# Optimization experiments

Hardware: AMD Instinct MI355X
Metric: run time of the kernel (lower is better)

The kernel has to match this reference:

```python
import jax, jax.numpy as jnp
import numpy as np


def setup_inputs() -> dict:
    key = jax.random.key(0)
    k1, k2, k3, k4 = jax.random.split(key, 4)
    b, c_in, t, h, w = 8, 64, 16, 64, 64
    c_out, kh, kw = 64, 3, 3
    x = jax.random.normal(k1, (b, c_in, t, h, w), dtype=jnp.float32)
    alpha = jax.random.uniform(k2, (b, c_in, t, 1, 1), dtype=jnp.float32)
    fan_in = c_in * kh * kw
    weight = jax.random.normal(k3, (c_out, c_in, kh, kw), dtype=jnp.float32) / np.sqrt(fan_in)
    bias = jax.random.normal(k4, (c_out,), dtype=jnp.float32) * 0.05
    return {"x": x, "alpha": alpha, "weight": weight, "bias": bias}


def reference(x, alpha, weight, bias):
    # x: (b, c_in, t, h, w); alpha: (b, c_in, t, 1, 1)
    # weight: (c_out, c_in, kh, kw); bias: (c_out,)
    b, c_in, t, h, w = x.shape
    c_out, _, kh, kw = weight.shape
    pad = ((kh // 2, kh // 2), (kw // 2, kw // 2))  # padding=1 for 3x3
    # per-(b,t) calibrated weights: alpha scales the c_in dim (cal_dim='cin')
    a = jnp.transpose(alpha[..., 0, 0], (0, 2, 1))          # (b, t, c_in)
    w_bt = a[:, :, None, :, None, None] * weight[None, None]  # (b, t, c_out, c_in, kh, kw)
    xs = jnp.transpose(x, (0, 2, 1, 3, 4)).reshape(b * t, 1, c_in, h, w)
    ws = w_bt.reshape(b * t, c_out, c_in, kh, kw)

    def conv_one(xi, wi):
        return jax.lax.conv_general_dilated(
            xi, wi, window_strides=(1, 1), padding=pad,
            dimension_numbers=("NCHW", "OIHW", "NCHW"))[0]

    out = jax.vmap(conv_one)(xs, ws)                          # (b*t, c_out, h, w)
    out = out + bias[None, :, None, None]
    out = out.reshape(b, t, c_out, h, w).transpose(0, 2, 1, 3, 4)
    return out  # (b, c_out, t, h, w)
```

## Files before the change

kernel.cpp:

```cpp
#include <hip/hip_runtime.h>


#define CIN  64
#define COUT 64
#define TT   16
#define BB   8
#define HH   64
#define WW   64

typedef __attribute__((ext_vector_type(8))) short bf16x8;
typedef __attribute__((ext_vector_type(4))) float f32x4;

__device__ __forceinline__ unsigned short f2bf(float f) {
    union { float f; unsigned u; } v; v.f = f;
    unsigned r = (v.u + 0x7FFF + ((v.u >> 16) & 1)) >> 16;
    return (unsigned short)r;
}

__global__ __launch_bounds__(256) void prep_w(const float* __restrict__ wgt,
                                              unsigned short* __restrict__ wb) {
    int idx = blockIdx.x * 256 + threadIdx.x;
    if (idx < COUT * CIN * 9) {
        int co  = idx / (CIN * 9);
        int r   = idx - co * (CIN * 9);
        int ci  = r / 9;
        int tap = r - ci * 9;
        int slot = (ci >> 3) ^ (co & 7);
        wb[((tap * COUT + co) * 8 + slot) * 8 + (ci & 7)] = f2bf(wgt[idx]);
    }
}

__global__ __launch_bounds__(512, 4) void conv3(const float* __restrict__ x,
                                                const float* __restrict__ alpha,
                                                const short* __restrict__ wb,
                                                const float* __restrict__ bias,
                                                float* __restrict__ out) {
    __shared__ __align__(16) short xs[6][66 * 64];
    __shared__ __align__(16) short wl[2][64 * 64];

    const int orig  = blockIdx.x;
    const int blk   = (orig & 7) * 256 + (orig >> 3);
    const int ytile = blk & 15;
    const int bt    = blk >> 4;
    const int t     = bt & 15;
    const int b     = bt >> 4;
    const int y0    = ytile * 4;
    const int tid   = threadIdx.x;
    const int wv    = tid >> 6;
    const int lane  = tid & 63;

    {
        const int cib = wv * 8;
        float a0 = alpha[(b * CIN + cib + 0) * TT + t];
        float a1 = alpha[(b * CIN + cib + 1) * TT + t];
        float a2 = alpha[(b * CIN + cib + 2) * TT + t];
        float a3 = alpha[(b * CIN + cib + 3) * TT + t];
        float a4 = alpha[(b * CIN + cib + 4) * TT + t];
        float a5 = alpha[(b * CIN + cib + 5) * TT + t];
        float a6 = alpha[(b * CIN + cib + 6) * TT + t];
        float a7 = alpha[(b * CIN + cib + 7) * TT + t];
        const float* xb = x + (size_t)((b * CIN + cib) * TT + t) * (HH * WW);
        const int slot = wv ^ (lane & 7);
        const int CI_STRIDE = TT * HH * WW;
#pragma unroll
        for (int r = 0; r < 6; ++r) {
            const int gy = y0 - 1 + r;
            int4 o = {0, 0, 0, 0};
            if ((unsigned)gy < HH) {
                const float* p = xb + gy * WW + lane;
                float v0 = p[0 * CI_STRIDE] * a0;
                float v1 = p[1 * CI_STRIDE] * a1;
                float v2 = p[2 * CI_STRIDE] * a2;
                float v3 = p[3 * CI_STRIDE] * a3;
                float v4 = p[4 * CI_STRIDE] * a4;
                float v5 = p[5 * CI_STRIDE] * a5;
                float v6 = p[6 * CI_STRIDE] * a6;
                float v7 = p[7 * CI_STRIDE] * a7;
                o.x = (int)f2bf(v0) | ((int)f2bf(v1) << 16);
                o.y = (int)f2bf(v2) | ((int)f2bf(v3) << 16);
                o.z = (int)f2bf(v4) | ((int)f2bf(v5) << 16);
                o.w = (int)f2bf(v6) | ((int)f2bf(v7) << 16);
            }
            *(int4*)(xs[r] + (lane + 1) * 64 + slot * 8) = o;
            if (lane < 2) {
                int4 z = {0, 0, 0, 0};
                *(int4*)(xs[r] + lane * 65 * 64 + wv * 8) = z;
            }
        }
    }
    ((int4*)wl[0])[tid] = ((const int4*)wb)[tid];
    __syncthreads();

    f32x4 acc[4][2] = {};
    const int ywave = wv >> 1;
    const int wseg  = (wv & 1) * 32;
    const int co_l  = lane & 15;
    const int kg    = lane >> 4;

    for (int tap = 0; tap < 9; ++tap) {
        const int cur = tap & 1;
        int4 wp;
        if (tap < 8)
            wp = ((const int4*)(wb + (tap + 1) * 4096))[tid];
        const int ky = tap / 3;
        const int dx = (tap - 3 * ky) - 1;
        const short* xrow = xs[ywave + ky];
        const short* wcur = wl[cur];

#pragma unroll
        for (int kc = 0; kc < 2; ++kc) {
            const int g = kc * 4 + kg;
            bf16x8 af[4];
#pragma unroll
            for (int m = 0; m < 4; ++m) {
                int co   = m * 16 + co_l;
                int slot = g ^ (co & 7);
                af[m] = *(const bf16x8*)(wcur + co * 64 + slot * 8);
            }
            bf16x8 bfr[2];
#pragma unroll
            for (int nt = 0; nt < 2; ++nt) {
                int w    = wseg + nt * 16 + co_l;
                int wx   = w + dx;
                int slot = g ^ (wx & 7);
                bfr[nt] = *(const bf16x8*)(xrow + (wx + 1) * 64 + slot * 8);
            }
#pragma unroll
            for (int m = 0; m < 4; ++m)
#pragma unroll
                for (int nt = 0; nt < 2; ++nt)
                    acc[m][nt] = __builtin_amdgcn_mfma_f32_16x16x32_bf16(
                        af[m], bfr[nt], acc[m][nt], 0, 0, 0);
        }

        if (tap < 8)
            ((int4*)wl[cur ^ 1])[tid] = wp;
        __syncthreads();
    }

    const int y = y0 + ywave;
#pragma unroll
    for (int m = 0; m < 4; ++m) {
#pragma unroll
        for (int r = 0; r < 4; ++r) {
            int co = m * 16 + kg * 4 + r;
            float bv = bias[co];
            float* op = out + (size_t)(((b * COUT + co) * TT + t) * HH + y) * WW;
#pragma unroll
            for (int nt = 0; nt < 2; ++nt) {
                int w = wseg + nt * 16 + co_l;
                op[w] = acc[m][nt][r] + bv;
            }
        }
    }
}

extern "C" void kernel_launch(void* const* d_in, const int* in_sizes, int n_in,
                              void* d_out, int out_size, void* d_ws, size_t ws_size,
                              hipStream_t stream) {
    const float* x      = (const float*)d_in[0];
    const float* alpha  = (const float*)d_in[1];
    const float* weight = (const float*)d_in[2];
    const float* bias   = (const float*)d_in[3];
    float* out          = (float*)d_out;

    unsigned short* wb = (unsigned short*)d_ws;

    hipLaunchKernelGGL(prep_w, dim3(144), dim3(256), 0, stream, weight, wb);
    hipLaunchKernelGGL(conv3, dim3(BB * TT * (HH / 4)), dim3(512), 0, stream,
                       x, alpha, (const short*)wb, bias, out);
}
```

Baseline: 261.2 us.

## Hold per-wave weight fragments in registers and drop the LDS weight pipeline

Weights are repacked in MFMA fragment order, and each wave now owns one 16-output-channel quarter. It loads all 9 taps of its weight fragments into registers once, so the per-tap LDS weight double buffer and its nine barriers go away. The wave-to-output mapping changes from 4 co-tiles × 2 w-tiles to 1 co-tile × 2 rows × 4 w-tiles, so the main loop only reads activations from LDS. This costs 72 extra VGPRs per thread for the weights, which may strain the 4-blocks-per-CU launch bound or cause spills.

```diff
diff --git a/kernel.cpp b/kernel.cpp
--- a/kernel.cpp
+++ b/kernel.cpp
@@ -25,18 +25,21 @@
         int r   = idx - co * (CIN * 9);
         int ci  = r / 9;
         int tap = r - ci * 9;
-        int slot = (ci >> 3) ^ (co & 7);
-        wb[((tap * COUT + co) * 8 + slot) * 8 + (ci & 7)] = f2bf(wgt[idx]);
+        int q    = co >> 4;
+        int co_l = co & 15;
+        int kc   = ci >> 5;
+        int kg   = (ci >> 3) & 3;
+        int e    = ci & 7;
+        wb[(((((q * 9 + tap) * 2 + kc) * 4 + kg) * 16) + co_l) * 8 + e] = f2bf(wgt[idx]);
     }
 }
 
-__global__ __launch_bounds__(512, 4) void conv3(const float* __restrict__ x,
+__global__ __launch_bounds__(512, 4) void conv4(const float* __restrict__ x,
                                                 const float* __restrict__ alpha,
                                                 const short* __restrict__ wb,
                                                 const float* __restrict__ bias,
                                                 float* __restrict__ out) {
-    __shared__ __align__(16) short xs[6][66 * 64];
-    __shared__ __align__(16) short wl[2][64 * 64];
+    __shared__ __align__(16) short xs[6 * 66 * 64];
 
     const int orig  = blockIdx.x;
     const int blk   = (orig & 7) * 256 + (orig >> 3);
@@ -48,6 +51,17 @@
     const int tid   = threadIdx.x;
     const int wv    = tid >> 6;
     const int lane  = tid & 63;
+    const int co_l  = lane & 15;
+    const int kg    = lane >> 4;
+    const int q     = wv & 3;
+    const int ph    = wv >> 2;
+
+    bf16x8 wreg[9][2];
+#pragma unroll
+    for (int tap = 0; tap < 9; ++tap)
+#pragma unroll
+        for (int kc = 0; kc < 2; ++kc)
+            wreg[tap][kc] = *(const bf16x8*)(wb + (((q * 9 + tap) * 2 + kc) * 64 + lane) * 8);
 
     {
         const int cib = wv * 8;
@@ -81,76 +95,56 @@
                 o.z = (int)f2bf(v4) | ((int)f2bf(v5) << 16);
                 o.w = (int)f2bf(v6) | ((int)f2bf(v7) << 16);
             }
-            *(int4*)(xs[r] + (lane + 1) * 64 + slot * 8) = o;
+            *(int4*)(xs + r * 4224 + (lane + 1) * 64 + slot * 8) = o;
             if (lane < 2) {
                 int4 z = {0, 0, 0, 0};
-                *(int4*)(xs[r] + lane * 65 * 64 + wv * 8) = z;
+                *(int4*)(xs + r * 4224 + lane * 65 * 64 + wv * 8) = z;
             }
         }
     }
-    ((int4*)wl[0])[tid] = ((const int4*)wb)[tid];
     __syncthreads();
 
-    f32x4 acc[4][2] = {};
-    const int ywave = wv >> 1;
-    const int wseg  = (wv & 1) * 32;
-    const int co_l  = lane & 15;
-    const int kg    = lane >> 4;
-
-    for (int tap = 0; tap < 9; ++tap) {
-        const int cur = tap & 1;
-        int4 wp;
-        if (tap < 8)
-            wp = ((const int4*)(wb + (tap + 1) * 4096))[tid];
-        const int ky = tap / 3;
-        const int dx = (tap - 3 * ky) - 1;
-        const short* xrow = xs[ywave + ky];
-        const short* wcur = wl[cur];
+    f32x4 acc[2][4] = {};
+    int si[3][2];
+#pragma unroll
+    for (int dxi = 0; dxi < 3; ++dxi)
+#pragma unroll
+        for (int kc = 0; kc < 2; ++kc) {
+            int wx = co_l + dxi - 1;
+            si[dxi][kc] = (wx + 1) * 64 + (((kc * 4 + kg) ^ (wx & 7)) * 8);
+        }
 
 #pragma unroll
+    for (int tap = 0; tap < 9; ++tap) {
+        const int ky  = tap / 3;
+        const int dxi = tap - 3 * ky;
+        const int rb  = (ph * 2 + ky) * 4224;
+#pragma unroll
         for (int kc = 0; kc < 2; ++kc) {
-            const int g = kc * 4 + kg;
-            bf16x8 af[4];
 #pragma unroll
-            for (int m = 0; m < 4; ++m) {
-                int co   = m * 16 + co_l;
-                int slot = g ^ (co & 7);
-                af[m] = *(const bf16x8*)(wcur + co * 64 + slot * 8);
+            for (int r = 0; r < 2; ++r) {
+                const short* rowp = xs + rb + r * 4224 + si[dxi][kc];
+#pragma unroll
+                for (int n = 0; n < 4; ++n) {
+                    bf16x8 bfr = *(const bf16x8*)(rowp + n * 1024);
+                    acc[r][n] = __builtin_amdgcn_mfma_f32_16x16x32_bf16(
+                        wreg[tap][kc], bfr, acc[r][n], 0, 0, 0);
+                }
             }
-            bf16x8 bfr[2];
-#pragma unroll
-            for (int nt = 0; nt < 2; ++nt) {
-                int w    = wseg + nt * 16 + co_l;
-                int wx   = w + dx;
-                int slot = g ^ (wx & 7);
-                bfr[nt] = *(const bf16x8*)(xrow + (wx + 1) * 64 + slot * 8);
-            }
-#pragma unroll
-            for (int m = 0; m < 4; ++m)
-#pragma unroll
-                for (int nt = 0; nt < 2; ++nt)
-                    acc[m][nt] = __builtin_amdgcn_mfma_f32_16x16x32_bf16(
-                        af[m], bfr[nt], acc[m][nt], 0, 0, 0);
         }
-
-        if (tap < 8)
-            ((int4*)wl[cur ^ 1])[tid] = wp;
-        __syncthreads();
     }
 
-    const int y = y0 + ywave;
 #pragma unroll
-    for (int m = 0; m < 4; ++m) {
+    for (int r = 0; r < 2; ++r) {
+        const int y = y0 + ph * 2 + r;
 #pragma unroll
-        for (int r = 0; r < 4; ++r) {
-            int co = m * 16 + kg * 4 + r;
-            float bv = bias[co];
+        for (int rr = 0; rr < 4; ++rr) {
+            const int co = q * 16 + kg * 4 + rr;
+            const float bv = bias[co];
             float* op = out + (size_t)(((b * COUT + co) * TT + t) * HH + y) * WW;
 #pragma unroll
-            for (int nt = 0; nt < 2; ++nt) {
-                int w = wseg + nt * 16 + co_l;
-                op[w] = acc[m][nt][r] + bv;
-            }
+            for (int n = 0; n < 4; ++n)
+                op[n * 16 + co_l] = acc[r][n][rr] + bv;
         }
     }
 }
@@ -167,6 +161,6 @@
     unsigned short* wb = (unsigned short*)d_ws;
 
     hipLaunchKernelGGL(prep_w, dim3(144), dim3(256), 0, stream, weight, wb);
-    hipLaunchKernelGGL(conv3, dim3(BB * TT * (HH / 4)), dim3(512), 0, stream,
+    hipLaunchKernelGGL(conv4, dim3(BB * TT * (HH / 4)), dim3(512), 0, stream,
                        x, alpha, (const short*)wb, bias, out);
 }
```

Measured after the change: 269.7 us. 3.2% more time.
